# Kernel tuning notes

Measured on AMD Instinct MI355X. Metric: run time of the kernel, lower is better.

## Reference

```python
import jax, jax.numpy as jnp
import numpy as np

N = 50000      # num nodes
E = 800000     # num edges (before self-loops)
IN = 128       # in_channels
H = 8          # heads (layer 1)
C = 32         # hidden_channels per head
OUT = 64       # out_channels


def setup_inputs() -> dict:
    key = jax.random.key(0)
    ks = jax.random.split(key, 9)
    x = jax.random.normal(ks[0], (N, IN), dtype=jnp.float32)
    edge_index = jax.random.randint(ks[1], (2, E), 0, N, dtype=jnp.int64)
    # layer 1 params (heads=H, concat=True)
    W1 = jax.random.normal(ks[2], (IN, H * C), dtype=jnp.float32) / np.float32(np.sqrt(IN))
    a_src1 = jax.random.normal(ks[3], (H, C), dtype=jnp.float32) / np.float32(np.sqrt(C))
    a_dst1 = jax.random.normal(ks[4], (H, C), dtype=jnp.float32) / np.float32(np.sqrt(C))
    b1 = jnp.zeros((H * C,), dtype=jnp.float32)
    # layer 2 params (heads=1, concat=False)
    W2 = jax.random.normal(ks[5], (H * C, OUT), dtype=jnp.float32) / np.float32(np.sqrt(H * C))
    a_src2 = jax.random.normal(ks[6], (1, OUT), dtype=jnp.float32) / np.float32(np.sqrt(OUT))
    a_dst2 = jax.random.normal(ks[7], (1, OUT), dtype=jnp.float32) / np.float32(np.sqrt(OUT))
    b2 = jnp.zeros((OUT,), dtype=jnp.float32)
    return {"x": x, "edge_index": edge_index,
            "W1": W1, "a_src1": a_src1, "a_dst1": a_dst1, "b1": b1,
            "W2": W2, "a_src2": a_src2, "a_dst2": a_dst2, "b2": b2}


def _gat_layer(x, src, dst, W, a_src, a_dst, b, concat):
    # PyG GATConv (eval mode): linear -> per-head attention logits ->
    # LeakyReLU(0.2) -> segment softmax over destination -> scatter-add.
    Hh, Cc = a_src.shape
    h = (x @ W).reshape(x.shape[0], Hh, Cc)          # [N, H, C]
    al = jnp.sum(h * a_src[None], axis=-1)           # [N, H]
    ar = jnp.sum(h * a_dst[None], axis=-1)           # [N, H]
    e = jax.nn.leaky_relu(al[src] + ar[dst], 0.2)    # [E', H]
    m = jax.ops.segment_max(e, dst, num_segments=N)  # per-dst max (self-loops guarantee coverage)
    p = jnp.exp(e - m[dst])
    s = jax.ops.segment_sum(p, dst, num_segments=N)
    alpha = p / (s[dst] + 1e-16)                     # [E', H]
    out = jax.ops.segment_sum(h[src] * alpha[:, :, None], dst, num_segments=N)  # [N, H, C]
    if concat:
        return out.reshape(N, Hh * Cc) + b
    return jnp.mean(out, axis=1) + b


def reference(x, edge_index, W1, a_src1, a_dst1, b1, W2, a_src2, a_dst2, b2):
    loops = jnp.arange(N, dtype=edge_index.dtype)
    src = jnp.concatenate([edge_index[0], loops])    # add_self_loops=True
    dst = jnp.concatenate([edge_index[1], loops])
    h = _gat_layer(x, src, dst, W1, a_src1, a_dst1, b1, True)   # [N, H*C]
    h = jax.nn.elu(h)                                            # dropout inactive in eval
    return _gat_layer(h, src, dst, W2, a_src2, a_dst2, b2, False)  # [N, OUT]
```

## Files before the change

### kernel.cpp

```cpp
#include <hip/hip_runtime.h>
#include <cstdint>

#define N_NODES 50000
#define N_EDGES 800000
#define E_TOT   (N_EDGES + N_NODES)
#define IN_CH   128
#define HEADS   8
#define CCH     32
#define HC      256
#define OUTC    64

typedef unsigned short ushort_t;
typedef __attribute__((ext_vector_type(8))) short bf16x8;
typedef __attribute__((ext_vector_type(8))) unsigned short u16x8;
typedef __attribute__((ext_vector_type(4))) float f32x4;

static __device__ __forceinline__ unsigned short f2bf(float f) {
    unsigned u = __float_as_uint(f);
    u = u + 0x7fffu + ((u >> 16) & 1u);
    return (unsigned short)(u >> 16);
}
static __device__ __forceinline__ float bf2f(unsigned short h) {
    return __uint_as_float((unsigned)h << 16);
}
static __device__ __forceinline__ unsigned pack2(float lo, float hi) {
    return (unsigned)f2bf(lo) | ((unsigned)f2bf(hi) << 16);
}
static __device__ __forceinline__ float lrexp(float v) {
    v = v > 0.f ? v : 0.2f * v;
    return expf(v);
}
static __device__ __forceinline__ bf16x8 cvt8(float4 lo, float4 hi) {
    bf16x8 r;
    r[0] = (short)f2bf(lo.x); r[1] = (short)f2bf(lo.y);
    r[2] = (short)f2bf(lo.z); r[3] = (short)f2bf(lo.w);
    r[4] = (short)f2bf(hi.x); r[5] = (short)f2bf(hi.y);
    r[6] = (short)f2bf(hi.z); r[7] = (short)f2bf(hi.w);
    return r;
}

__global__ __launch_bounds__(256) void prep_kernel(
        const int* __restrict__ ei, int* __restrict__ deg,
        const float* __restrict__ W1, const float* __restrict__ W2,
        ushort_t* __restrict__ W1f, ushort_t* __restrict__ W2f) {
    int t = blockIdx.x * 256 + threadIdx.x;
    if (t < 32768) {
        int j = t & 7, lane = (t >> 3) & 63, f = t >> 9;
        int nt = f >> 2, kk = f & 3;
        int k = kk * 32 + (lane >> 4) * 8 + j;
        int n = (nt >> 1) * 32 + 2 * (lane & 15) + (nt & 1);
        W1f[t] = f2bf(W1[k * HC + n]);
    } else if (t < 32768 + 16384) {
        int u = t - 32768;
        int j = u & 7, lane = (u >> 3) & 63, f = u >> 9;
        int nt = f >> 3, kk = f & 7;
        int k = kk * 32 + (lane >> 4) * 8 + j;
        int n = (nt >> 1) * 32 + 2 * (lane & 15) + (nt & 1);
        W2f[u] = f2bf(W2[k * OUTC + n]);
    }
    if (t < E_TOT) {
        int dv = (t < N_EDGES) ? ei[N_EDGES + t] : (t - N_EDGES);
        atomicAdd(&deg[dv], 1);
    }
}

__global__ __launch_bounds__(1024) void scan1_kernel(
        const int* __restrict__ deg, int* __restrict__ inc, int* __restrict__ bsum) {
    __shared__ int sh[1024];
    const int tid = threadIdx.x;
    const int i = blockIdx.x * 1024 + tid;
    sh[tid] = (i < N_NODES) ? deg[i] : 0;
    __syncthreads();
    for (int o = 1; o < 1024; o <<= 1) {
        int t = (tid >= o) ? sh[tid - o] : 0;
        __syncthreads();
        sh[tid] += t;
        __syncthreads();
    }
    if (i < N_NODES) inc[i] = sh[tid];
    if (tid == 1023) bsum[blockIdx.x] = sh[1023];
}

#define NSCAN_BLOCKS ((N_NODES + 1023) / 1024)
__global__ __launch_bounds__(256) void finalize_kernel(
        const int* __restrict__ inc, const int* __restrict__ bsum,
        int* __restrict__ rowstart, int* __restrict__ cursor) {
    __shared__ int pref[NSCAN_BLOCKS];
    if (threadIdx.x == 0) {
        int acc = 0;
        #pragma unroll 7
        for (int k = 0; k < NSCAN_BLOCKS; ++k) { pref[k] = acc; acc += bsum[k]; }
    }
    __syncthreads();
    int i = blockIdx.x * 256 + threadIdx.x;
    if (i >= N_NODES) return;
    int v = inc[i] + pref[i >> 10];
    rowstart[i + 1] = v;
    if (i + 1 < N_NODES) cursor[i + 1] = v;
    if (i == 0) { rowstart[0] = 0; cursor[0] = 0; }
}

__global__ __launch_bounds__(256) void scatter_kernel(
        const int* __restrict__ ei, int* __restrict__ cursor, int* __restrict__ col) {
    int e = blockIdx.x * 256 + threadIdx.x;
    if (e >= E_TOT) return;
    int sv, dv;
    if (e < N_EDGES) { sv = ei[e]; dv = ei[N_EDGES + e]; }
    else             { sv = dv = e - N_EDGES; }
    int pos = atomicAdd(&cursor[dv], 1);
    col[pos] = sv;
}

__global__ __launch_bounds__(256) void gemm1_mfma(
        const float* __restrict__ x, const ushort_t* __restrict__ W1f,
        const float* __restrict__ a_src, const float* __restrict__ a_dst,
        ushort_t* __restrict__ h1b, float* __restrict__ al, float* __restrict__ ar) {
    const int lane = threadIdx.x & 63;
    const int wv   = threadIdx.x >> 6;
    const int base = blockIdx.x * 64 + wv * 16;
    if (base >= N_NODES) return;
    const int am = base + (lane & 15);
    const int rm = am < N_NODES ? am : N_NODES - 1;

    bf16x8 a[4];
    const float* xr = &x[(size_t)rm * IN_CH + (lane >> 4) * 8];
    #pragma unroll
    for (int kk = 0; kk < 4; ++kk) {
        float4 lo = *(const float4*)&xr[kk * 32];
        float4 hi = *(const float4*)&xr[kk * 32 + 4];
        a[kk] = cvt8(lo, hi);
    }

    f32x4 acc[16];
    #pragma unroll
    for (int nt = 0; nt < 16; ++nt) acc[nt] = (f32x4){0.f, 0.f, 0.f, 0.f};

    const bf16x8* bp = (const bf16x8*)W1f;
    #pragma unroll
    for (int nt = 0; nt < 16; ++nt) {
        #pragma unroll
        for (int kk = 0; kk < 4; ++kk)
            acc[nt] = __builtin_amdgcn_mfma_f32_16x16x32_bf16(
                a[kk], bp[(nt * 4 + kk) * 64 + lane], acc[nt], 0, 0, 0);
    }

    #pragma unroll
    for (int r = 0; r < 4; ++r) {
        int node = base + (lane >> 4) * 4 + r;
        if (node < N_NODES) {
            unsigned* op = (unsigned*)&h1b[(size_t)node * HC + 2 * (lane & 15)];
            #pragma unroll
            for (int t = 0; t < 8; ++t)
                op[t * 16] = pack2(acc[2 * t][r], acc[2 * t + 1][r]);
        }
    }

    float asv[16], adv[16];
    #pragma unroll
    for (int nt = 0; nt < 16; ++nt) {
        int n = (nt >> 1) * 32 + 2 * (lane & 15) + (nt & 1);
        asv[nt] = a_src[n];
        adv[nt] = a_dst[n];
    }
    #pragma unroll
    for (int h = 0; h < HEADS; ++h) {
        #pragma unroll
        for (int r = 0; r < 4; ++r) {
            float s = acc[2 * h][r] * asv[2 * h] + acc[2 * h + 1][r] * asv[2 * h + 1];
            float d = acc[2 * h][r] * adv[2 * h] + acc[2 * h + 1][r] * adv[2 * h + 1];
            s += __shfl_xor(s, 1, 64); s += __shfl_xor(s, 2, 64);
            s += __shfl_xor(s, 4, 64); s += __shfl_xor(s, 8, 64);
            d += __shfl_xor(d, 1, 64); d += __shfl_xor(d, 2, 64);
            d += __shfl_xor(d, 4, 64); d += __shfl_xor(d, 8, 64);
            int node = base + (lane >> 4) * 4 + r;
            if ((lane & 15) == 0 && node < N_NODES) {
                al[node * HEADS + h] = s;
                ar[node * HEADS + h] = d;
            }
        }
    }
}

__global__ __launch_bounds__(256) void aggr1_csr(
        const int* __restrict__ rowstart, const int* __restrict__ col,
        const float* __restrict__ al, const float* __restrict__ ar,
        const unsigned short* __restrict__ h1b, const float* __restrict__ b1,
        unsigned short* __restrict__ out1b) {
    const int lane = threadIdx.x & 63;
    const int d = blockIdx.x * 4 + (threadIdx.x >> 6);
    if (d >= N_NODES) return;
    const int beg = rowstart[d], end = rowstart[d + 1];

    const int eq = lane >> 3;
    const int eh = lane & 7;
    const float ar_eh = ar[d * HEADS + eh];
    const int half = lane >> 5;
    const int L    = lane & 31;
    const int hh   = L >> 2;

    float dsum = 0.f;
    float acc8[8] = {0.f,0.f,0.f,0.f,0.f,0.f,0.f,0.f};

    for (int i = beg; i < end; i += 8) {
        const int e = i + eq;
        const int sv_e = col[e < end ? e : end - 1];
        const float ex = (e < end) ? lrexp(al[sv_e * HEADS + eh] + ar_eh) : 0.f;
        dsum += ex;
        #pragma unroll
        for (int q = 0; q < 4; ++q) {
            const int src = (2 * q + half) * 8;
            const int   sq = __shfl(sv_e, src, 64);
            const float wq = __shfl(ex, src + hh, 64);
            const u16x8 v = *(const u16x8*)&h1b[(size_t)sq * HC + L * 8];
            #pragma unroll
            for (int j = 0; j < 8; ++j) acc8[j] += wq * bf2f(v[j]);
        }
    }
    dsum += __shfl_xor(dsum, 8, 64);
    dsum += __shfl_xor(dsum, 16, 64);
    dsum += __shfl_xor(dsum, 32, 64);
    const float inv = 1.f / (__shfl(dsum, hh, 64) + 1e-16f);
    #pragma unroll
    for (int j = 0; j < 8; ++j) acc8[j] *= inv;
    #pragma unroll
    for (int j = 0; j < 8; ++j) acc8[j] += __shfl_xor(acc8[j], 32, 64);

    if (half == 0) {
        const float4 b0 = *(const float4*)&b1[L * 8];
        const float4 b4 = *(const float4*)&b1[L * 8 + 4];
        float bb[8] = {b0.x, b0.y, b0.z, b0.w, b4.x, b4.y, b4.z, b4.w};
        u16x8 ov;
        #pragma unroll
        for (int j = 0; j < 8; ++j) {
            float v = acc8[j] + bb[j];
            v = v > 0.f ? v : expf(v) - 1.f;
            ov[j] = f2bf(v);
        }
        *(u16x8*)&out1b[(size_t)d * HC + L * 8] = ov;
    }
}

__global__ __launch_bounds__(256) void gemm2_mfma(
        const ushort_t* __restrict__ hinb, const ushort_t* __restrict__ W2f,
        const float* __restrict__ a_src, const float* __restrict__ a_dst,
        ushort_t* __restrict__ h2b, float* __restrict__ al, float* __restrict__ ar) {
    const int lane = threadIdx.x & 63;
    const int wv   = threadIdx.x >> 6;
    const int base = blockIdx.x * 64 + wv * 16;
    if (base >= N_NODES) return;
    const int am = base + (lane & 15);
    const int rm = am < N_NODES ? am : N_NODES - 1;

    bf16x8 a[8];
    const bf16x8* ap = (const bf16x8*)&hinb[(size_t)rm * HC];
    #pragma unroll
    for (int kk = 0; kk < 8; ++kk)
        a[kk] = ap[kk * 4 + (lane >> 4)];

    f32x4 acc[4];
    #pragma unroll
    for (int nt = 0; nt < 4; ++nt) acc[nt] = (f32x4){0.f, 0.f, 0.f, 0.f};

    const bf16x8* bp = (const bf16x8*)W2f;
    #pragma unroll
    for (int nt = 0; nt < 4; ++nt) {
        #pragma unroll
        for (int kk = 0; kk < 8; ++kk)
            acc[nt] = __builtin_amdgcn_mfma_f32_16x16x32_bf16(
                a[kk], bp[(nt * 8 + kk) * 64 + lane], acc[nt], 0, 0, 0);
    }

    #pragma unroll
    for (int r = 0; r < 4; ++r) {
        int node = base + (lane >> 4) * 4 + r;
        if (node < N_NODES) {
            unsigned* op = (unsigned*)&h2b[(size_t)node * OUTC + 2 * (lane & 15)];
            #pragma unroll
            for (int t = 0; t < 2; ++t)
                op[t * 16] = pack2(acc[2 * t][r], acc[2 * t + 1][r]);
        }
    }

    float asv[4], adv[4];
    #pragma unroll
    for (int nt = 0; nt < 4; ++nt) {
        int n = (nt >> 1) * 32 + 2 * (lane & 15) + (nt & 1);
        asv[nt] = a_src[n];
        adv[nt] = a_dst[n];
    }
    #pragma unroll
    for (int r = 0; r < 4; ++r) {
        float s = 0.f, d = 0.f;
        #pragma unroll
        for (int nt = 0; nt < 4; ++nt) {
            s += acc[nt][r] * asv[nt];
            d += acc[nt][r] * adv[nt];
        }
        s += __shfl_xor(s, 1, 64); s += __shfl_xor(s, 2, 64);
        s += __shfl_xor(s, 4, 64); s += __shfl_xor(s, 8, 64);
        d += __shfl_xor(d, 1, 64); d += __shfl_xor(d, 2, 64);
        d += __shfl_xor(d, 4, 64); d += __shfl_xor(d, 8, 64);
        int node = base + (lane >> 4) * 4 + r;
        if ((lane & 15) == 0 && node < N_NODES) { al[node] = s; ar[node] = d; }
    }
}

__global__ __launch_bounds__(256) void aggr2_csr(
        const int* __restrict__ rowstart, const int* __restrict__ col,
        const float* __restrict__ al, const float* __restrict__ ar,
        const unsigned short* __restrict__ h2b, const float* __restrict__ b2,
        float* __restrict__ out) {
    const int lane = threadIdx.x & 63;
    const int d = blockIdx.x * 4 + (threadIdx.x >> 6);
    if (d >= N_NODES) return;
    const int beg = rowstart[d], end = rowstart[d + 1];
    const float ard = ar[d];

    const int e8 = lane & 7;
    const int g  = lane >> 4;
    const int L  = lane & 15;

    float dsum = 0.f;
    float4 acc = {0.f, 0.f, 0.f, 0.f};

    for (int i = beg; i < end; i += 8) {
        const int e = i + e8;
        const int sv_e = col[e < end ? e : end - 1];
        const float ex = (e < end) ? lrexp(al[sv_e] + ard) : 0.f;
        dsum += ex;
        #pragma unroll
        for (int q = 0; q < 2; ++q) {
            const int slot = q * 4 + g;
            const int   sq = __shfl(sv_e, slot, 64);
            const float wq = __shfl(ex, slot, 64);
            const ushort4 v = *(const ushort4*)&h2b[(size_t)sq * OUTC + L * 4];
            acc.x += wq * bf2f(v.x); acc.y += wq * bf2f(v.y);
            acc.z += wq * bf2f(v.z); acc.w += wq * bf2f(v.w);
        }
    }
    dsum += __shfl_xor(dsum, 1, 64);
    dsum += __shfl_xor(dsum, 2, 64);
    dsum += __shfl_xor(dsum, 4, 64);
    const float inv = 1.f / (dsum + 1e-16f);
    acc.x *= inv; acc.y *= inv; acc.z *= inv; acc.w *= inv;
    #pragma unroll
    for (int o = 16; o < 64; o <<= 1) {
        acc.x += __shfl_xor(acc.x, o, 64);
        acc.y += __shfl_xor(acc.y, o, 64);
        acc.z += __shfl_xor(acc.z, o, 64);
        acc.w += __shfl_xor(acc.w, o, 64);
    }
    if (g == 0) {
        const float4 bb = *(const float4*)&b2[L * 4];
        float4 ov = { acc.x + bb.x, acc.y + bb.y, acc.z + bb.z, acc.w + bb.w };
        *(float4*)&out[(size_t)d * OUTC + L * 4] = ov;
    }
}

extern "C" void kernel_launch(void* const* d_in, const int* in_sizes, int n_in,
                              void* d_out, int out_size, void* d_ws, size_t ws_size,
                              hipStream_t stream) {
    const float* x      = (const float*)d_in[0];
    const int*   ei     = (const int*)  d_in[1];
    const float* W1     = (const float*)d_in[2];
    const float* a_src1 = (const float*)d_in[3];
    const float* a_dst1 = (const float*)d_in[4];
    const float* b1     = (const float*)d_in[5];
    const float* W2     = (const float*)d_in[6];
    const float* a_src2 = (const float*)d_in[7];
    const float* a_dst2 = (const float*)d_in[8];
    const float* b2     = (const float*)d_in[9];
    float* out = (float*)d_out;

    char* p = (char*)d_ws;
    ushort_t* h1b   = (ushort_t*)p; p += (size_t)N_NODES * HC * 2;
    ushort_t* out1b = (ushort_t*)p; p += (size_t)N_NODES * HC * 2;
    ushort_t* h2b   = (ushort_t*)p; p += (size_t)N_NODES * OUTC * 2;
    ushort_t* W1f  = (ushort_t*)p; p += 32768 * 2;
    ushort_t* W2f  = (ushort_t*)p; p += 16384 * 2;
    float* al1  = (float*)p;  p += (size_t)N_NODES * HEADS * sizeof(float);
    float* ar1  = (float*)p;  p += (size_t)N_NODES * HEADS * sizeof(float);
    float* al2  = (float*)p;  p += (size_t)N_NODES * sizeof(float);
    float* ar2  = (float*)p;  p += (size_t)N_NODES * sizeof(float);
    int* deg      = (int*)p;  p += (size_t)N_NODES * sizeof(int);
    int* inc      = (int*)p;  p += (size_t)N_NODES * sizeof(int);
    int* bsum     = (int*)p;  p += (size_t)NSCAN_BLOCKS * sizeof(int);
    int* rowstart = (int*)p;  p += (size_t)(N_NODES + 1) * sizeof(int);
    int* cursor   = (int*)p;  p += (size_t)N_NODES * sizeof(int);
    int* col      = (int*)p;  p += (size_t)E_TOT * sizeof(int);

    hipMemsetAsync(deg, 0, (size_t)N_NODES * sizeof(int), stream);
    prep_kernel    <<<(E_TOT + 255)/256, 256, 0, stream>>>(ei, deg, W1, W2, W1f, W2f);
    scan1_kernel   <<<NSCAN_BLOCKS, 1024, 0, stream>>>(deg, inc, bsum);
    finalize_kernel<<<(N_NODES + 255)/256, 256, 0, stream>>>(inc, bsum, rowstart, cursor);
    scatter_kernel <<<(E_TOT + 255)/256, 256, 0, stream>>>(ei, cursor, col);

    gemm1_mfma <<<(N_NODES + 63)/64, 256, 0, stream>>>(x, W1f, a_src1, a_dst1, h1b, al1, ar1);
    aggr1_csr  <<<(N_NODES + 3)/4, 256, 0, stream>>>(rowstart, col, al1, ar1, h1b, b1, out1b);

    gemm2_mfma <<<(N_NODES + 63)/64, 256, 0, stream>>>(out1b, W2f, a_src2, a_dst2, h2b, al2, ar2);
    aggr2_csr  <<<(N_NODES + 3)/4, 256, 0, stream>>>(rowstart, col, al2, ar2, h2b, b2, out);
}
```

Before: 254.1 us.

## Fuse CSR construction into a single cooperative kernel with grid syncs

Replaces the memset plus four separate CSR-building launches (degree count, block scan, finalize, scatter) with one cooperative kernel of 1024 blocks that uses grid.sync between phases. The scan now uses 256-wide blocks. The goal is to remove launch overhead and inter-kernel gaps for the small preprocessing stages. The cost is grid-wide barriers, a grid-stride loop over edges with fewer threads, and reliance on every block being co-resident.

```diff
diff --git a/kernel.cpp b/kernel.cpp
--- a/kernel.cpp
+++ b/kernel.cpp
@@ -1,5 +1,8 @@
 #include <hip/hip_runtime.h>
+#include <hip/hip_cooperative_groups.h>
 #include <cstdint>
+
+namespace cg = cooperative_groups;
 
 #define N_NODES 50000
 #define N_EDGES 800000
@@ -9,6 +12,8 @@
 #define CCH     32
 #define HC      256
 #define OUTC    64
+#define COOP_BLOCKS 1024
+#define NSCANB  196
 
 typedef unsigned short ushort_t;
 typedef __attribute__((ext_vector_type(8))) short bf16x8;
@@ -39,76 +44,80 @@
     return r;
 }
 
-__global__ __launch_bounds__(256) void prep_kernel(
-        const int* __restrict__ ei, int* __restrict__ deg,
+__global__ __launch_bounds__(256) void csr_coop(
+        const int* __restrict__ ei,
         const float* __restrict__ W1, const float* __restrict__ W2,
-        ushort_t* __restrict__ W1f, ushort_t* __restrict__ W2f) {
-    int t = blockIdx.x * 256 + threadIdx.x;
-    if (t < 32768) {
-        int j = t & 7, lane = (t >> 3) & 63, f = t >> 9;
+        ushort_t* __restrict__ W1f, ushort_t* __restrict__ W2f,
+        int* __restrict__ deg, int* __restrict__ inc, int* __restrict__ bsum,
+        int* __restrict__ rowstart, int* __restrict__ cursor,
+        int* __restrict__ col) {
+    cg::grid_group grid = cg::this_grid();
+    __shared__ int sh[256];
+    __shared__ int pref[NSCANB];
+    const int tid = blockIdx.x * 256 + threadIdx.x;
+    const int nth = COOP_BLOCKS * 256;
+
+    for (int i = tid; i < N_NODES; i += nth) deg[i] = 0;
+    if (tid < 32768) {
+        int j = tid & 7, lane = (tid >> 3) & 63, f = tid >> 9;
         int nt = f >> 2, kk = f & 3;
         int k = kk * 32 + (lane >> 4) * 8 + j;
         int n = (nt >> 1) * 32 + 2 * (lane & 15) + (nt & 1);
-        W1f[t] = f2bf(W1[k * HC + n]);
-    } else if (t < 32768 + 16384) {
-        int u = t - 32768;
+        W1f[tid] = f2bf(W1[k * HC + n]);
+    } else if (tid < 32768 + 16384) {
+        int u = tid - 32768;
         int j = u & 7, lane = (u >> 3) & 63, f = u >> 9;
         int nt = f >> 3, kk = f & 7;
         int k = kk * 32 + (lane >> 4) * 8 + j;
         int n = (nt >> 1) * 32 + 2 * (lane & 15) + (nt & 1);
         W2f[u] = f2bf(W2[k * OUTC + n]);
     }
-    if (t < E_TOT) {
-        int dv = (t < N_EDGES) ? ei[N_EDGES + t] : (t - N_EDGES);
+    grid.sync();
+
+    for (int e = tid; e < E_TOT; e += nth) {
+        int dv = (e < N_EDGES) ? ei[N_EDGES + e] : (e - N_EDGES);
         atomicAdd(&deg[dv], 1);
     }
-}
-
-__global__ __launch_bounds__(1024) void scan1_kernel(
-        const int* __restrict__ deg, int* __restrict__ inc, int* __restrict__ bsum) {
-    __shared__ int sh[1024];
-    const int tid = threadIdx.x;
-    const int i = blockIdx.x * 1024 + tid;
-    sh[tid] = (i < N_NODES) ? deg[i] : 0;
-    __syncthreads();
-    for (int o = 1; o < 1024; o <<= 1) {
-        int t = (tid >= o) ? sh[tid - o] : 0;
+    grid.sync();
+
+    if (blockIdx.x < NSCANB) {
+        int i = blockIdx.x * 256 + threadIdx.x;
+        sh[threadIdx.x] = (i < N_NODES) ? deg[i] : 0;
         __syncthreads();
-        sh[tid] += t;
+        for (int o = 1; o < 256; o <<= 1) {
+            int t = (threadIdx.x >= o) ? sh[threadIdx.x - o] : 0;
+            __syncthreads();
+            sh[threadIdx.x] += t;
+            __syncthreads();
+        }
+        if (i < N_NODES) inc[i] = sh[threadIdx.x];
+        if (threadIdx.x == 255) bsum[blockIdx.x] = sh[255];
+    }
+    grid.sync();
+
+    if (blockIdx.x < NSCANB) {
+        if (threadIdx.x == 0) {
+            int acc = 0;
+            for (int k = 0; k < NSCANB; ++k) { pref[k] = acc; acc += bsum[k]; }
+        }
         __syncthreads();
-    }
-    if (i < N_NODES) inc[i] = sh[tid];
-    if (tid == 1023) bsum[blockIdx.x] = sh[1023];
-}
-
-#define NSCAN_BLOCKS ((N_NODES + 1023) / 1024)
-__global__ __launch_bounds__(256) void finalize_kernel(
-        const int* __restrict__ inc, const int* __restrict__ bsum,
-        int* __restrict__ rowstart, int* __restrict__ cursor) {
-    __shared__ int pref[NSCAN_BLOCKS];
-    if (threadIdx.x == 0) {
-        int acc = 0;
-        #pragma unroll 7
-        for (int k = 0; k < NSCAN_BLOCKS; ++k) { pref[k] = acc; acc += bsum[k]; }
-    }
-    __syncthreads();
-    int i = blockIdx.x * 256 + threadIdx.x;
-    if (i >= N_NODES) return;
-    int v = inc[i] + pref[i >> 10];
-    rowstart[i + 1] = v;
-    if (i + 1 < N_NODES) cursor[i + 1] = v;
-    if (i == 0) { rowstart[0] = 0; cursor[0] = 0; }
-}
-
-__global__ __launch_bounds__(256) void scatter_kernel(
-        const int* __restrict__ ei, int* __restrict__ cursor, int* __restrict__ col) {
-    int e = blockIdx.x * 256 + threadIdx.x;
-    if (e >= E_TOT) return;
-    int sv, dv;
-    if (e < N_EDGES) { sv = ei[e]; dv = ei[N_EDGES + e]; }
-    else             { sv = dv = e - N_EDGES; }
-    int pos = atomicAdd(&cursor[dv], 1);
-    col[pos] = sv;
+        int i = blockIdx.x * 256 + threadIdx.x;
+        if (i < N_NODES) {
+            int v = inc[i] + pref[blockIdx.x];
+            rowstart[i + 1] = v;
+            if (i + 1 < N_NODES) cursor[i + 1] = v;
+            if (i == 0) { rowstart[0] = 0; cursor[0] = 0; }
+        }
+    }
+    grid.sync();
+
+    for (int e = tid; e < E_TOT; e += nth) {
+        int sv, dv;
+        if (e < N_EDGES) { sv = ei[e]; dv = ei[N_EDGES + e]; }
+        else             { sv = dv = e - N_EDGES; }
+        int pos = atomicAdd(&cursor[dv], 1);
+        col[pos] = sv;
+    }
 }
 
 __global__ __launch_bounds__(256) void gemm1_mfma(
@@ -360,8 +369,8 @@
 extern "C" void kernel_launch(void* const* d_in, const int* in_sizes, int n_in,
                               void* d_out, int out_size, void* d_ws, size_t ws_size,
                               hipStream_t stream) {
+    const int*   ei     = (const int*)  d_in[1];
     const float* x      = (const float*)d_in[0];
-    const int*   ei     = (const int*)  d_in[1];
     const float* W1     = (const float*)d_in[2];
     const float* a_src1 = (const float*)d_in[3];
     const float* a_dst1 = (const float*)d_in[4];
@@ -384,16 +393,20 @@
     float* ar2  = (float*)p;  p += (size_t)N_NODES * sizeof(float);
     int* deg      = (int*)p;  p += (size_t)N_NODES * sizeof(int);
     int* inc      = (int*)p;  p += (size_t)N_NODES * sizeof(int);
-    int* bsum     = (int*)p;  p += (size_t)NSCAN_BLOCKS * sizeof(int);
+    int* bsum     = (int*)p;  p += (size_t)NSCANB * sizeof(int);
     int* rowstart = (int*)p;  p += (size_t)(N_NODES + 1) * sizeof(int);
     int* cursor   = (int*)p;  p += (size_t)N_NODES * sizeof(int);
     int* col      = (int*)p;  p += (size_t)E_TOT * sizeof(int);
 
-    hipMemsetAsync(deg, 0, (size_t)N_NODES * sizeof(int), stream);
-    prep_kernel    <<<(E_TOT + 255)/256, 256, 0, stream>>>(ei, deg, W1, W2, W1f, W2f);
-    scan1_kernel   <<<NSCAN_BLOCKS, 1024, 0, stream>>>(deg, inc, bsum);
-    finalize_kernel<<<(N_NODES + 255)/256, 256, 0, stream>>>(inc, bsum, rowstart, cursor);
-    scatter_kernel <<<(E_TOT + 255)/256, 256, 0, stream>>>(ei, cursor, col);
+    {
+        void* args[] = {
+            (void*)&ei, (void*)&W1, (void*)&W2, (void*)&W1f, (void*)&W2f,
+            (void*)&deg, (void*)&inc, (void*)&bsum,
+            (void*)&rowstart, (void*)&cursor, (void*)&col
+        };
+        hipLaunchCooperativeKernel((void*)csr_coop, dim3(COOP_BLOCKS), dim3(256),
+                                   args, 0, stream);
+    }
 
     gemm1_mfma <<<(N_NODES + 63)/64, 256, 0, stream>>>(x, W1f, a_src1, a_dst1, h1b, al1, ar1);
     aggr1_csr  <<<(N_NODES + 3)/4, 256, 0, stream>>>(rowstart, col, al1, ar1, h1b, b1, out1b);
```

Measured after the change: 637.3 us. 151% more time.
